# Kernel optimization log

Hardware: AMD Instinct MI355X
Metric: run time of the kernel (lower is better)

The kernel has to match this reference:

```python
import jax, jax.numpy as jnp
import numpy as np

N, E, EMB, G, L = 30000, 480000, 256, 512, 3
AVOCAB, BVOCAB, EDIM = 128, 16, 3
NEG_SLOPE = 0.2


def setup_inputs() -> dict:
    key = jax.random.key(0)
    ks = jax.random.split(key, 20)
    s = 0.05
    x = jax.random.randint(ks[0], (N, 9), 0, AVOCAB)
    edge_index = jax.random.randint(ks[1], (2, E), 0, N)
    edge_attr = jax.random.randint(ks[2], (E, 3), 0, BVOCAB)
    batch = jnp.sort(jax.random.randint(ks[3], (N,), 0, G))
    return {
        "x": x, "edge_index": edge_index, "edge_attr": edge_attr, "batch": batch,
        # AtomEncoder: 9 embedding tables summed -> [N, EMB]
        "atom_emb": jax.random.normal(ks[4], (9, AVOCAB, EMB)) * s,
        # BondEncoder per layer: 3 tables summed -> [E, 3]
        "bond_emb": jax.random.normal(ks[5], (L, 3, BVOCAB, EDIM)) * s,
        # GATConv per layer (heads=1): lin W, att vectors, lin_edge, bias
        "W": jax.random.normal(ks[6], (L, EMB, EMB)) * s,
        "att_src": jax.random.normal(ks[7], (L, EMB)) * s,
        "att_dst": jax.random.normal(ks[8], (L, EMB)) * s,
        "We": jax.random.normal(ks[9], (L, EDIM, EMB)) * s,
        "att_edge": jax.random.normal(ks[10], (L, EMB)) * s,
        "bias": jnp.zeros((L, EMB)),
        # head MLP: Linear(EMB,EMB) -> Linear(EMB,1), no activation between
        "W1": jax.random.normal(ks[11], (EMB, EMB)) * s,
        "b1": jnp.zeros((EMB,)),
        "W2": jax.random.normal(ks[12], (EMB, 1)) * s,
        "b2": jnp.zeros((1,)),
    }


def _gat_conv(h, src, dst, e_enc, W, a_s, a_d, We, a_e, b):
    # PyG GATConv, heads=1, add_self_loops=True, fill_value='mean'.
    # self-loop edge_attr = mean of incoming edge attrs per node (0 if none)
    deg = jax.ops.segment_sum(jnp.ones((E,), h.dtype), dst, num_segments=N)
    loop_attr = jax.ops.segment_sum(e_enc, dst, num_segments=N) / jnp.clip(deg, 1.0)[:, None]
    e_all = jnp.concatenate([e_enc, loop_attr], axis=0)          # [E+N, 3]
    loops = jnp.arange(N, dtype=src.dtype)
    src_a = jnp.concatenate([src, loops])
    dst_a = jnp.concatenate([dst, loops])
    xl = h @ W                                                    # [N, C]
    alpha = (xl @ a_s)[src_a] + (xl @ a_d)[dst_a] + (e_all @ We) @ a_e  # [E+N]
    alpha = jnp.where(alpha >= 0, alpha, NEG_SLOPE * alpha)       # leaky_relu
    # segment softmax over destination (every node has a self loop -> nonempty)
    m = jax.ops.segment_max(alpha, dst_a, num_segments=N)
    p = jnp.exp(alpha - m[dst_a])
    denom = jax.ops.segment_sum(p, dst_a, num_segments=N)
    w = p / denom[dst_a]
    out = jax.ops.segment_sum(w[:, None] * xl[src_a], dst_a, num_segments=N)
    return out + b


def reference(x, edge_index, edge_attr, batch, atom_emb, bond_emb, W, att_src,
              att_dst, We, att_edge, bias, W1, b1, W2, b2):
    src, dst = edge_index[0], edge_index[1]
    # AtomEncoder: sum of 9 feature embeddings
    h = sum(atom_emb[i][x[:, i]] for i in range(9))               # [N, EMB]
    for l in range(L):
        e_enc = sum(bond_emb[l, j][edge_attr[:, j]] for j in range(3))  # [E, 3]
        hc = _gat_conv(h, src, dst, e_enc, W[l], att_src[l], att_dst[l],
                       We[l], att_edge[l], bias[l])
        if l < L - 1:
            hc = jax.nn.relu(hc)
        h = hc + h  # residual (dropout is identity in eval)
    # global mean pool
    cnt = jax.ops.segment_sum(jnp.ones((N,), h.dtype), batch, num_segments=G)
    hg = jax.ops.segment_sum(h, batch, num_segments=G) / jnp.clip(cnt, 1.0)[:, None]
    return (hg @ W1 + b1) @ W2 + b2                               # [G, 1]
```

## Files before the change

kernel.cpp:

```cpp
#include <hip/hip_runtime.h>
#include <hip/hip_bf16.h>

#define NN   30000
#define NE   480000
#define EMBD 256
#define NG   512
#define NLAY 3
#define LEAK 0.2f
#define NBLK_SCAN 118

typedef __attribute__((ext_vector_type(8))) short bf16x8;
typedef __attribute__((ext_vector_type(4))) float f32x4;
typedef __attribute__((ext_vector_type(4))) unsigned short us4;
typedef __attribute__((ext_vector_type(8))) unsigned short us8;

__device__ __forceinline__ float bf2f(unsigned short u) {
  union { unsigned int i; float f; } v; v.i = ((unsigned int)u) << 16; return v.f;
}
__device__ __forceinline__ unsigned short f2bf(float f) {
  union { float f; unsigned int i; } v; v.f = f;
  unsigned int u = v.i;
  u += 0x7fffu + ((u >> 16) & 1u);
  return (unsigned short)(u >> 16);
}
__device__ __forceinline__ float rdw(const void* p, size_t i, int f32) {
  return f32 ? ((const float*)p)[i] : bf2f(((const unsigned short*)p)[i]);
}

__global__ __launch_bounds__(256) void k_sniff_multi(const unsigned short* __restrict__ w,
                                                     int* cnt) {
  __shared__ int sh;
  if (threadIdx.x == 0) sh = 0;
  __syncthreads();
  int local = 0;
  for (int i = (blockIdx.x * 256 + threadIdx.x) * 2; i < 65536; i += 16 * 256 * 2) {
    unsigned short u = w[i];
    if (((u >> 7) & 0xFF) == 0xFF) local++;
  }
  atomicAdd(&sh, local);
  __syncthreads();
  if (threadIdx.x == 0 && sh) atomicAdd(cnt, sh);
}

__global__ __launch_bounds__(256) void k_dots(const void* __restrict__ We,
                                              const void* __restrict__ ae,
                                              const void* __restrict__ W1,
                                              const void* __restrict__ b1,
                                              const void* __restrict__ W2,
                                              const void* __restrict__ b2,
                                              const int* __restrict__ cntp,
                                              float* __restrict__ wa_all,
                                              float* __restrict__ v,
                                              float* __restrict__ c0) {
  int f32 = (*cntp >= 4) ? 1 : 0;
  int wid  = blockIdx.x * 4 + (threadIdx.x >> 6);
  int lane = threadIdx.x & 63;
  if (wid >= 266) return;
  float s = 0.f;
  if (wid < 256) {
    for (int c = lane; c < 256; c += 64)
      s += rdw(W1, (size_t)wid*256 + c, f32) * rdw(W2, c, f32);
  } else if (wid < 265) {
    int t = wid - 256;
    int l = t / 3, j = t % 3;
    for (int c = lane; c < 256; c += 64)
      s += rdw(We, (size_t)l*768 + j*256 + c, f32) * rdw(ae, (size_t)l*256 + c, f32);
  } else {
    for (int c = lane; c < 256; c += 64)
      s += rdw(b1, c, f32) * rdw(W2, c, f32);
  }
  #pragma unroll
  for (int o = 32; o > 0; o >>= 1) s += __shfl_down(s, o);
  if (lane == 0) {
    if (wid < 256)      v[wid] = s;
    else if (wid < 265) wa_all[wid - 256] = s;
    else                *c0 = s + rdw(b2, 0, f32);
  }
}


__global__ void k_hist(const int* __restrict__ dst, int* cnt_i) {
  int e = blockIdx.x * 256 + threadIdx.x;
  if (e >= NE) return;
  atomicAdd(&cnt_i[dst[e]], 1);
}

__global__ __launch_bounds__(256) void k_scan_part(const int* __restrict__ cnt_i,
                                                   int* row_ptr, int* part) {
  __shared__ int sh[256];
  int b = blockIdx.x, t = threadIdx.x;
  int i = b * 256 + t;
  int v = (i < NN) ? cnt_i[i] : 0;
  sh[t] = v;
  __syncthreads();
  for (int off = 1; off < 256; off <<= 1) {
    int tmp = (t >= off) ? sh[t - off] : 0;
    __syncthreads();
    sh[t] += tmp;
    __syncthreads();
  }
  if (i < NN) row_ptr[i] = sh[t] - v;
  if (t == 255) part[b] = sh[255];
}

__global__ __launch_bounds__(128) void k_scan_mid(const int* __restrict__ part,
                                                  int* __restrict__ offs) {
  __shared__ int sh[128];
  int t = threadIdx.x;
  int v = (t < NBLK_SCAN) ? part[t] : 0;
  sh[t] = v;
  __syncthreads();
  for (int off = 1; off < 128; off <<= 1) {
    int tmp = (t >= off) ? sh[t - off] : 0;
    __syncthreads();
    sh[t] += tmp;
    __syncthreads();
  }
  if (t < NBLK_SCAN) offs[t] = sh[t] - v;
}

__global__ void k_scan_add(int* row_ptr, const int* __restrict__ offs, int* cursor) {
  int b = blockIdx.x, t = threadIdx.x;
  int i = b * 256 + t;
  if (i < NN) {
    int v = row_ptr[i] + offs[b];
    row_ptr[i] = v;
    cursor[i]  = v;
  }
  if (i == 0) row_ptr[NN] = NE;
}

__global__ void k_fill(const int* __restrict__ src, const int* __restrict__ dst,
                       int* cursor, int* col_src, int* col_eid) {
  int e = blockIdx.x * 256 + threadIdx.x;
  if (e >= NE) return;
  int pos = atomicAdd(&cursor[dst[e]], 1);
  col_src[pos] = src[e];
  col_eid[pos] = e;
}


__global__ __launch_bounds__(256) void k_prep(const void* __restrict__ W,
                                              unsigned short* __restrict__ Wt,
                                              const int* __restrict__ eattr,
                                              const int* __restrict__ col_eid,
                                              const void* __restrict__ bemb,
                                              const float* __restrict__ wa_all,
                                              float* __restrict__ we_csr,
                                              const int* __restrict__ cntp) {
  int f32 = (*cntp >= 4) ? 1 : 0;
  int b = blockIdx.x;
  if (b < 768) {
    int t = b * 256 + threadIdx.x;
    int l = t >> 16;
    int k = (t >> 8) & 255;
    int c = t & 255;
    Wt[(l << 16) + (c << 8) + k] = f2bf(rdw(W, t, f32));
  } else {
    int j = (b - 768) * 256 + threadIdx.x;
    if (j >= NE) return;
    int e = col_eid[j];
    int a0 = eattr[e*3], a1 = eattr[e*3+1], a2 = eattr[e*3+2];
    #pragma unroll
    for (int l = 0; l < NLAY; ++l) {
      size_t lb = (size_t)l * 144;
      float e0 = rdw(bemb, lb + (0*16+a0)*3+0, f32) + rdw(bemb, lb + (1*16+a1)*3+0, f32)
               + rdw(bemb, lb + (2*16+a2)*3+0, f32);
      float e1 = rdw(bemb, lb + (0*16+a0)*3+1, f32) + rdw(bemb, lb + (1*16+a1)*3+1, f32)
               + rdw(bemb, lb + (2*16+a2)*3+1, f32);
      float e2 = rdw(bemb, lb + (0*16+a0)*3+2, f32) + rdw(bemb, lb + (1*16+a1)*3+2, f32)
               + rdw(bemb, lb + (2*16+a2)*3+2, f32);
      we_csr[(size_t)l*NE + j] = e0*wa_all[l*3+0] + e1*wa_all[l*3+1] + e2*wa_all[l*3+2];
    }
  }
}

__global__ void k_atom_enc(const int* __restrict__ x, const void* __restrict__ emb,
                           float* __restrict__ h, unsigned short* __restrict__ hbf,
                           const int* __restrict__ cntp) {
  int f32 = (*cntp >= 4) ? 1 : 0;
  int n = blockIdx.x, c = threadIdx.x;
  float s = 0.f;
  #pragma unroll
  for (int i = 0; i < 9; ++i) {
    int xi = x[n * 9 + i];
    s += rdw(emb, (size_t)(i * 128 + xi) * 256 + c, f32);
  }
  h[n * 256 + c] = s;
  hbf[n * 256 + c] = f2bf(s);
}


__global__ __launch_bounds__(256) void k_gemm_fused(const unsigned short* __restrict__ A,
                                                    const unsigned short* __restrict__ Bt,
                                                    const void* __restrict__ as_w,
                                                    const void* __restrict__ ad_w, int l,
                                                    unsigned short* __restrict__ xlbf,
                                                    float* __restrict__ as_,
                                                    float* __restrict__ ad_,
                                                    const int* __restrict__ cntp) {
  __shared__ unsigned short xtile[16][256];
  __shared__ float sred[4][4][4], dred[4][4][4];
  int b = blockIdx.x;
  int w = threadIdx.x >> 6;
  int lane = threadIdx.x & 63;
  int m0 = b * 16;
  int c0 = w * 64;
  int lr = lane & 15;
  int g  = lane >> 4;
  int lk = g * 8;
  f32x4 acc0 = {0.f,0.f,0.f,0.f}, acc1 = {0.f,0.f,0.f,0.f};
  f32x4 acc2 = {0.f,0.f,0.f,0.f}, acc3 = {0.f,0.f,0.f,0.f};
  const unsigned short* arow = A  + (size_t)(m0 + lr) * 256 + lk;
  const unsigned short* b0   = Bt + (size_t)(c0 + lr) * 256 + lk;
  #pragma unroll
  for (int k = 0; k < 256; k += 32) {
    bf16x8 a = *(const bf16x8*)(arow + k);
    acc0 = __builtin_amdgcn_mfma_f32_16x16x32_bf16(a, *(const bf16x8*)(b0 + k),          acc0, 0,0,0);
    acc1 = __builtin_amdgcn_mfma_f32_16x16x32_bf16(a, *(const bf16x8*)(b0 + 16*256 + k), acc1, 0,0,0);
    acc2 = __builtin_amdgcn_mfma_f32_16x16x32_bf16(a, *(const bf16x8*)(b0 + 32*256 + k), acc2, 0,0,0);
    acc3 = __builtin_amdgcn_mfma_f32_16x16x32_bf16(a, *(const bf16x8*)(b0 + 48*256 + k), acc3, 0,0,0);
  }
  int f32 = (*cntp >= 4) ? 1 : 0;
  float asw0 = rdw(as_w, (size_t)l*256 + c0 + lr +  0, f32);
  float asw1 = rdw(as_w, (size_t)l*256 + c0 + lr + 16, f32);
  float asw2 = rdw(as_w, (size_t)l*256 + c0 + lr + 32, f32);
  float asw3 = rdw(as_w, (size_t)l*256 + c0 + lr + 48, f32);
  float adw0 = rdw(ad_w, (size_t)l*256 + c0 + lr +  0, f32);
  float adw1 = rdw(ad_w, (size_t)l*256 + c0 + lr + 16, f32);
  float adw2 = rdw(ad_w, (size_t)l*256 + c0 + lr + 32, f32);
  float adw3 = rdw(ad_w, (size_t)l*256 + c0 + lr + 48, f32);
  #pragma unroll
  for (int r = 0; r < 4; ++r) {
    float sv = acc0[r]*asw0 + acc1[r]*asw1 + acc2[r]*asw2 + acc3[r]*asw3;
    float dv = acc0[r]*adw0 + acc1[r]*adw1 + acc2[r]*adw2 + acc3[r]*adw3;
    #pragma unroll
    for (int o = 1; o < 16; o <<= 1) { sv += __shfl_xor(sv, o); dv += __shfl_xor(dv, o); }
    if (lr == 0) { sred[w][g][r] = sv; dred[w][g][r] = dv; }
    int row = g*4 + r;
    xtile[row][c0 + lr +  0] = f2bf(acc0[r]);
    xtile[row][c0 + lr + 16] = f2bf(acc1[r]);
    xtile[row][c0 + lr + 32] = f2bf(acc2[r]);
    xtile[row][c0 + lr + 48] = f2bf(acc3[r]);
  }
  __syncthreads();
  int t = threadIdx.x;
  if (t < 16) {
    int gg = t >> 2, rr = t & 3;
    float s = sred[0][gg][rr] + sred[1][gg][rr] + sred[2][gg][rr] + sred[3][gg][rr];
    float d = dred[0][gg][rr] + dred[1][gg][rr] + dred[2][gg][rr] + dred[3][gg][rr];
    as_[m0 + gg*4 + rr] = s;
    ad_[m0 + gg*4 + rr] = d;
  }
  {
    int row = t >> 4;
    int seg = t & 15;
    us8* dstp = (us8*)(xlbf + (size_t)(m0 + row) * 256);
    const us8* srcp = (const us8*)&xtile[row][0];
    dstp[seg]      = srcp[seg];
    dstp[seg + 16] = srcp[seg + 16];
  }
}

__global__ __launch_bounds__(256) void k_fused(const int* __restrict__ row_ptr,
                                               const int* __restrict__ col_src,
                                               const float* __restrict__ we_csr,
                                               const float* __restrict__ as_,
                                               const float* __restrict__ ad_,
                                               const unsigned short* __restrict__ xlbf,
                                               const void* __restrict__ bias, int l,
                                               float* __restrict__ h,
                                               unsigned short* __restrict__ hbf,
                                               int do_relu, const int* __restrict__ cntp) {
  int n = blockIdx.x * 4 + (threadIdx.x >> 6);
  int lane = threadIdx.x & 63;
  int beg = row_ptr[n], end = row_ptr[n+1];
  int deg = end - beg;
  float ad_n = ad_[n];

  float m = -1e30f, dsum = 0.f, wesum = 0.f;
  float ax = 0.f, ay = 0.f, az = 0.f, aw = 0.f;

  for (int cb = beg; cb < end; cb += 64) {
    int j = cb + lane;
    bool valid = (j < end);
    int s = valid ? col_src[j] : 0;
    float we = valid ? we_csr[j] : 0.f;
    wesum += we;
    float a;
    if (valid) {
      a = as_[s] + ad_n + we;
      a = (a >= 0.f) ? a : LEAK * a;
    } else {
      a = -1e30f;
    }
    float cm = a;
    #pragma unroll
    for (int o = 32; o > 0; o >>= 1) cm = fmaxf(cm, __shfl_xor(cm, o));
    float m_new = fmaxf(m, cm);
    float r = __expf(m - m_new);
    float p = valid ? __expf(a - m_new) : 0.f;
    float cs = p;
    #pragma unroll
    for (int o = 32; o > 0; o >>= 1) cs += __shfl_xor(cs, o);
    dsum = dsum * r + cs;
    ax *= r; ay *= r; az *= r; aw *= r;
    m = m_new;
    int cl = end - cb; if (cl > 64) cl = 64;
    for (int jj = 0; jj < cl; ++jj) {
      float w  = __shfl(p, jj);
      int   ss = __shfl(s, jj);
      us4 xv = *(const us4*)(xlbf + (size_t)ss*256 + lane*4);
      ax += w*bf2f(xv.x); ay += w*bf2f(xv.y);
      az += w*bf2f(xv.z); aw += w*bf2f(xv.w);
    }
  }
  #pragma unroll
  for (int o = 32; o > 0; o >>= 1) wesum += __shfl_xor(wesum, o);

  float a_self = as_[n] + ad_n + wesum / fmaxf((float)deg, 1.f);
  a_self = (a_self >= 0.f) ? a_self : LEAK * a_self;
  float m_f = fmaxf(m, a_self);
  float r = __expf(m - m_f);
  float p_self = __expf(a_self - m_f);
  dsum = dsum * r + p_self;
  ax *= r; ay *= r; az *= r; aw *= r;
  {
    us4 xv = *(const us4*)(xlbf + (size_t)n*256 + lane*4);
    ax += p_self*bf2f(xv.x); ay += p_self*bf2f(xv.y);
    az += p_self*bf2f(xv.z); aw += p_self*bf2f(xv.w);
  }
  float inv_d = 1.f / dsum;
  ax *= inv_d; ay *= inv_d; az *= inv_d; aw *= inv_d;

  int f32 = (*cntp >= 4) ? 1 : 0;
  int c0 = lane * 4;
  ax += rdw(bias, (size_t)l*256 + c0+0, f32);
  ay += rdw(bias, (size_t)l*256 + c0+1, f32);
  az += rdw(bias, (size_t)l*256 + c0+2, f32);
  aw += rdw(bias, (size_t)l*256 + c0+3, f32);
  if (do_relu) {
    ax = fmaxf(ax, 0.f); ay = fmaxf(ay, 0.f);
    az = fmaxf(az, 0.f); aw = fmaxf(aw, 0.f);
  }
  float* hp = h + (size_t)n*256 + c0;
  float4 hv = *(const float4*)hp;
  float h0 = ax + hv.x, h1 = ay + hv.y, h2 = az + hv.z, h3 = aw + hv.w;
  *(float4*)hp = make_float4(h0, h1, h2, h3);
  us4 q = { f2bf(h0), f2bf(h1), f2bf(h2), f2bf(h3) };
  *(us4*)(hbf + (size_t)n*256 + c0) = q;
}


__global__ __launch_bounds__(256) void k_pool_head(const float* __restrict__ h,
                                                   const int* __restrict__ batch,
                                                   const float* __restrict__ v,
                                                   const float* __restrict__ c0,
                                                   void* __restrict__ out,
                                                   const int* __restrict__ cntp) {
  int g = blockIdx.x;
  int lo = 0, hi = NN;
  while (lo < hi) { int mid = (lo + hi) >> 1; if (batch[mid] < g) lo = mid + 1; else hi = mid; }
  int start = lo;
  lo = 0; hi = NN;
  while (lo < hi) { int mid = (lo + hi) >> 1; if (batch[mid] < g + 1) lo = mid + 1; else hi = mid; }
  int endn = lo;

  int c = threadIdx.x;
  float s = 0.f;
  for (int n = start; n < endn; ++n) s += h[(size_t)n*256 + c];
  __shared__ float red[256];
  red[c] = s * v[c];
  __syncthreads();
  for (int off = 128; off > 0; off >>= 1) {
    if (c < off) red[c] += red[c + off];
    __syncthreads();
  }
  if (c == 0) {
    float cntf = (float)(endn - start);
    float val = red[0] / fmaxf(cntf, 1.f) + *c0;
    if (*cntp >= 4) ((float*)out)[g] = val;
    else            ((unsigned short*)out)[g] = f2bf(val);
  }
}

extern "C" void kernel_launch(void* const* d_in, const int* in_sizes, int n_in,
                              void* d_out, int out_size, void* d_ws, size_t ws_size,
                              hipStream_t stream) {
  const int* x     = (const int*)d_in[0];
  const int* eidx  = (const int*)d_in[1];
  const int* eattr = (const int*)d_in[2];
  const int* batch = (const int*)d_in[3];
  const void* atom_emb = d_in[4];
  const void* bond_emb = d_in[5];
  const void* W        = d_in[6];
  const void* att_src  = d_in[7];
  const void* att_dst  = d_in[8];
  const void* We       = d_in[9];
  const void* att_edge = d_in[10];
  const void* bias     = d_in[11];
  const void* W1 = d_in[12];
  const void* b1 = d_in[13];
  const void* W2 = d_in[14];
  const void* b2 = d_in[15];

  const int* src = eidx;
  const int* dst = eidx + NE;

  char* base = (char*)d_ws;
  size_t off = 0;
  auto alloc = [&](size_t bytes) -> char* {
    char* p = base + off; off += (bytes + 255) & ~(size_t)255; return p;
  };
  float* h    = (float*)alloc((size_t)NN*EMBD*4);
  unsigned short* xlbf = (unsigned short*)alloc((size_t)NN*EMBD*2);
  unsigned short* hbf  = (unsigned short*)alloc((size_t)NN*EMBD*2);
  unsigned short* wt   = (unsigned short*)alloc((size_t)NLAY*EMBD*EMBD*2);
  float* we_csr = (float*)alloc((size_t)NLAY*NE*4);
  float* as_   = (float*)alloc((size_t)NN*4);
  float* ad_   = (float*)alloc((size_t)NN*4);
  float* vvec  = (float*)alloc((size_t)EMBD*4);
  float* c0    = (float*)alloc(4);
  float* wa_all= (float*)alloc(64);
  int*   cnt   = (int*)alloc(4);
  int* cnt_i   = (int*)alloc((size_t)NN*4);
  int* row_ptr = (int*)alloc((size_t)(NN+1)*4);
  int* cursor  = (int*)alloc((size_t)NN*4);
  int* col_src = (int*)alloc((size_t)NE*4);
  int* col_eid = (int*)alloc((size_t)NE*4);
  int* part    = (int*)alloc((size_t)NBLK_SCAN*4);
  int* offs    = (int*)alloc((size_t)NBLK_SCAN*4);

  (void)hipMemsetAsync(cnt, 0, 4, stream);
  (void)hipMemsetAsync(cnt_i, 0, (size_t)NN*4, stream);
  k_sniff_multi<<<16, 256, 0, stream>>>((const unsigned short*)atom_emb, cnt);
  k_hist<<<(NE+255)/256, 256, 0, stream>>>(dst, cnt_i);
  k_scan_part<<<NBLK_SCAN, 256, 0, stream>>>(cnt_i, row_ptr, part);
  k_scan_mid<<<1, 128, 0, stream>>>(part, offs);
  k_scan_add<<<NBLK_SCAN, 256, 0, stream>>>(row_ptr, offs, cursor);
  k_fill<<<(NE+255)/256, 256, 0, stream>>>(src, dst, cursor, col_src, col_eid);
  k_dots<<<67, 256, 0, stream>>>(We, att_edge, W1, b1, W2, b2, cnt, wa_all, vvec, c0);
  k_atom_enc<<<NN, 256, 0, stream>>>(x, atom_emb, h, hbf, cnt);
  k_prep<<<768 + (NE+255)/256, 256, 0, stream>>>(W, wt, eattr, col_eid, bond_emb,
                                                 wa_all, we_csr, cnt);

  for (int l = 0; l < NLAY; ++l) {
    k_gemm_fused<<<NN/16, 256, 0, stream>>>(hbf, wt + (size_t)l*EMBD*EMBD,
                                            att_src, att_dst, l, xlbf, as_, ad_, cnt);
    k_fused<<<NN/4, 256, 0, stream>>>(row_ptr, col_src, we_csr + (size_t)l*NE,
                                      as_, ad_, xlbf, bias, l, h, hbf,
                                      (l < NLAY-1) ? 1 : 0, cnt);
  }

  k_pool_head<<<NG, 256, 0, stream>>>(h, batch, vvec, c0, d_out, cnt);
}
```

Before: 497.9 us.

## Merge setup kernels, enlarge GEMM row tile, drop online-max softmax rescaling

Independent setup kernels are merged into fewer launches: sniff with histogram, scan with dot products, and atom encoding with weight transpose. The GEMM now computes 48 rows per block, so each B-fragment load is reused across three row groups. The GAT aggregation drops the running-max online softmax and its per-chunk wave reductions, using clamped exponentials and a single reduction at the end. This removes launch overhead and per-chunk shuffle and rescale work, but the softmax is less numerically robust (clamping at ±60 changes results if logits get large), and it also unrolls the gather loop.

```diff
diff --git a/kernel.cpp b/kernel.cpp
--- a/kernel.cpp
+++ b/kernel.cpp
@@ -8,6 +8,7 @@
 #define NLAY 3
 #define LEAK 0.2f
 #define NBLK_SCAN 118
+#define GROWS 48
 
 typedef __attribute__((ext_vector_type(8))) short bf16x8;
 typedef __attribute__((ext_vector_type(4))) float f32x4;
@@ -27,80 +28,82 @@
   return f32 ? ((const float*)p)[i] : bf2f(((const unsigned short*)p)[i]);
 }
 
-__global__ __launch_bounds__(256) void k_sniff_multi(const unsigned short* __restrict__ w,
-                                                     int* cnt) {
-  __shared__ int sh;
-  if (threadIdx.x == 0) sh = 0;
-  __syncthreads();
-  int local = 0;
-  for (int i = (blockIdx.x * 256 + threadIdx.x) * 2; i < 65536; i += 16 * 256 * 2) {
-    unsigned short u = w[i];
-    if (((u >> 7) & 0xFF) == 0xFF) local++;
-  }
-  atomicAdd(&sh, local);
-  __syncthreads();
-  if (threadIdx.x == 0 && sh) atomicAdd(cnt, sh);
-}
-
-__global__ __launch_bounds__(256) void k_dots(const void* __restrict__ We,
-                                              const void* __restrict__ ae,
-                                              const void* __restrict__ W1,
-                                              const void* __restrict__ b1,
-                                              const void* __restrict__ W2,
-                                              const void* __restrict__ b2,
-                                              const int* __restrict__ cntp,
-                                              float* __restrict__ wa_all,
-                                              float* __restrict__ v,
-                                              float* __restrict__ c0) {
-  int f32 = (*cntp >= 4) ? 1 : 0;
-  int wid  = blockIdx.x * 4 + (threadIdx.x >> 6);
-  int lane = threadIdx.x & 63;
-  if (wid >= 266) return;
-  float s = 0.f;
-  if (wid < 256) {
-    for (int c = lane; c < 256; c += 64)
-      s += rdw(W1, (size_t)wid*256 + c, f32) * rdw(W2, c, f32);
-  } else if (wid < 265) {
-    int t = wid - 256;
-    int l = t / 3, j = t % 3;
-    for (int c = lane; c < 256; c += 64)
-      s += rdw(We, (size_t)l*768 + j*256 + c, f32) * rdw(ae, (size_t)l*256 + c, f32);
+__global__ __launch_bounds__(256) void k_sniff_hist(const unsigned short* __restrict__ w,
+                                                    int* cnt, const int* __restrict__ dst,
+                                                    int* cnt_i) {
+  int b = blockIdx.x;
+  if (b < 16) {
+    __shared__ int sh;
+    if (threadIdx.x == 0) sh = 0;
+    __syncthreads();
+    int local = 0;
+    for (int i = (b * 256 + threadIdx.x) * 2; i < 65536; i += 16 * 256 * 2) {
+      unsigned short u = w[i];
+      if (((u >> 7) & 0xFF) == 0xFF) local++;
+    }
+    atomicAdd(&sh, local);
+    __syncthreads();
+    if (threadIdx.x == 0 && sh) atomicAdd(cnt, sh);
   } else {
-    for (int c = lane; c < 256; c += 64)
-      s += rdw(b1, c, f32) * rdw(W2, c, f32);
-  }
-  #pragma unroll
-  for (int o = 32; o > 0; o >>= 1) s += __shfl_down(s, o);
-  if (lane == 0) {
-    if (wid < 256)      v[wid] = s;
-    else if (wid < 265) wa_all[wid - 256] = s;
-    else                *c0 = s + rdw(b2, 0, f32);
-  }
-}
-
-
-__global__ void k_hist(const int* __restrict__ dst, int* cnt_i) {
-  int e = blockIdx.x * 256 + threadIdx.x;
-  if (e >= NE) return;
-  atomicAdd(&cnt_i[dst[e]], 1);
-}
-
-__global__ __launch_bounds__(256) void k_scan_part(const int* __restrict__ cnt_i,
-                                                   int* row_ptr, int* part) {
-  __shared__ int sh[256];
-  int b = blockIdx.x, t = threadIdx.x;
-  int i = b * 256 + t;
-  int v = (i < NN) ? cnt_i[i] : 0;
-  sh[t] = v;
-  __syncthreads();
-  for (int off = 1; off < 256; off <<= 1) {
-    int tmp = (t >= off) ? sh[t - off] : 0;
-    __syncthreads();
-    sh[t] += tmp;
-    __syncthreads();
-  }
-  if (i < NN) row_ptr[i] = sh[t] - v;
-  if (t == 255) part[b] = sh[255];
+    int e = (b - 16) * 256 + threadIdx.x;
+    if (e < NE) atomicAdd(&cnt_i[dst[e]], 1);
+  }
+}
+
+__global__ __launch_bounds__(256) void k_scan_dots(const int* __restrict__ cnt_i,
+                                                   int* row_ptr, int* part,
+                                                   const void* __restrict__ We,
+                                                   const void* __restrict__ ae,
+                                                   const void* __restrict__ W1,
+                                                   const void* __restrict__ b1,
+                                                   const void* __restrict__ W2,
+                                                   const void* __restrict__ b2,
+                                                   const int* __restrict__ cntp,
+                                                   float* __restrict__ wa_all,
+                                                   float* __restrict__ v,
+                                                   float* __restrict__ c0) {
+  int b = blockIdx.x;
+  if (b < NBLK_SCAN) {
+    __shared__ int sh[256];
+    int t = threadIdx.x;
+    int i = b * 256 + t;
+    int val = (i < NN) ? cnt_i[i] : 0;
+    sh[t] = val;
+    __syncthreads();
+    for (int off = 1; off < 256; off <<= 1) {
+      int tmp = (t >= off) ? sh[t - off] : 0;
+      __syncthreads();
+      sh[t] += tmp;
+      __syncthreads();
+    }
+    if (i < NN) row_ptr[i] = sh[t] - val;
+    if (t == 255) part[b] = sh[255];
+  } else {
+    int f32 = (*cntp >= 4) ? 1 : 0;
+    int wid  = (b - NBLK_SCAN) * 4 + (threadIdx.x >> 6);
+    int lane = threadIdx.x & 63;
+    if (wid >= 266) return;
+    float s = 0.f;
+    if (wid < 256) {
+      for (int c = lane; c < 256; c += 64)
+        s += rdw(W1, (size_t)wid*256 + c, f32) * rdw(W2, c, f32);
+    } else if (wid < 265) {
+      int t = wid - 256;
+      int l = t / 3, j = t % 3;
+      for (int c = lane; c < 256; c += 64)
+        s += rdw(We, (size_t)l*768 + j*256 + c, f32) * rdw(ae, (size_t)l*256 + c, f32);
+    } else {
+      for (int c = lane; c < 256; c += 64)
+        s += rdw(b1, c, f32) * rdw(W2, c, f32);
+    }
+    #pragma unroll
+    for (int o = 32; o > 0; o >>= 1) s += __shfl_down(s, o);
+    if (lane == 0) {
+      if (wid < 256)      v[wid] = s;
+      else if (wid < 265) wa_all[wid - 256] = s;
+      else                *c0 = s + rdw(b2, 0, f32);
+    }
+  }
 }
 
 __global__ __launch_bounds__(128) void k_scan_mid(const int* __restrict__ part,
@@ -139,55 +142,56 @@
   col_eid[pos] = e;
 }
 
-
-__global__ __launch_bounds__(256) void k_prep(const void* __restrict__ W,
-                                              unsigned short* __restrict__ Wt,
-                                              const int* __restrict__ eattr,
-                                              const int* __restrict__ col_eid,
-                                              const void* __restrict__ bemb,
-                                              const float* __restrict__ wa_all,
-                                              float* __restrict__ we_csr,
-                                              const int* __restrict__ cntp) {
+__global__ __launch_bounds__(256) void k_atom_prep(const int* __restrict__ x,
+                                                   const void* __restrict__ emb,
+                                                   float* __restrict__ h,
+                                                   unsigned short* __restrict__ hbf,
+                                                   const void* __restrict__ W,
+                                                   unsigned short* __restrict__ Wt,
+                                                   const int* __restrict__ cntp) {
   int f32 = (*cntp >= 4) ? 1 : 0;
   int b = blockIdx.x;
-  if (b < 768) {
-    int t = b * 256 + threadIdx.x;
+  if (b < NN) {
+    int c = threadIdx.x;
+    float s = 0.f;
+    #pragma unroll
+    for (int i = 0; i < 9; ++i) {
+      int xi = x[b * 9 + i];
+      s += rdw(emb, (size_t)(i * 128 + xi) * 256 + c, f32);
+    }
+    h[(size_t)b * 256 + c] = s;
+    hbf[(size_t)b * 256 + c] = f2bf(s);
+  } else {
+    int t = (b - NN) * 256 + threadIdx.x;
     int l = t >> 16;
     int k = (t >> 8) & 255;
     int c = t & 255;
     Wt[(l << 16) + (c << 8) + k] = f2bf(rdw(W, t, f32));
-  } else {
-    int j = (b - 768) * 256 + threadIdx.x;
-    if (j >= NE) return;
-    int e = col_eid[j];
-    int a0 = eattr[e*3], a1 = eattr[e*3+1], a2 = eattr[e*3+2];
-    #pragma unroll
-    for (int l = 0; l < NLAY; ++l) {
-      size_t lb = (size_t)l * 144;
-      float e0 = rdw(bemb, lb + (0*16+a0)*3+0, f32) + rdw(bemb, lb + (1*16+a1)*3+0, f32)
-               + rdw(bemb, lb + (2*16+a2)*3+0, f32);
-      float e1 = rdw(bemb, lb + (0*16+a0)*3+1, f32) + rdw(bemb, lb + (1*16+a1)*3+1, f32)
-               + rdw(bemb, lb + (2*16+a2)*3+1, f32);
-      float e2 = rdw(bemb, lb + (0*16+a0)*3+2, f32) + rdw(bemb, lb + (1*16+a1)*3+2, f32)
-               + rdw(bemb, lb + (2*16+a2)*3+2, f32);
-      we_csr[(size_t)l*NE + j] = e0*wa_all[l*3+0] + e1*wa_all[l*3+1] + e2*wa_all[l*3+2];
-    }
-  }
-}
-
-__global__ void k_atom_enc(const int* __restrict__ x, const void* __restrict__ emb,
-                           float* __restrict__ h, unsigned short* __restrict__ hbf,
-                           const int* __restrict__ cntp) {
+  }
+}
+
+__global__ __launch_bounds__(256) void k_we(const int* __restrict__ eattr,
+                                            const int* __restrict__ col_eid,
+                                            const void* __restrict__ bemb,
+                                            const float* __restrict__ wa_all,
+                                            float* __restrict__ we_csr,
+                                            const int* __restrict__ cntp) {
   int f32 = (*cntp >= 4) ? 1 : 0;
-  int n = blockIdx.x, c = threadIdx.x;
-  float s = 0.f;
-  #pragma unroll
-  for (int i = 0; i < 9; ++i) {
-    int xi = x[n * 9 + i];
-    s += rdw(emb, (size_t)(i * 128 + xi) * 256 + c, f32);
-  }
-  h[n * 256 + c] = s;
-  hbf[n * 256 + c] = f2bf(s);
+  int j = blockIdx.x * 256 + threadIdx.x;
+  if (j >= NE) return;
+  int e = col_eid[j];
+  int a0 = eattr[e*3], a1 = eattr[e*3+1], a2 = eattr[e*3+2];
+  #pragma unroll
+  for (int l = 0; l < NLAY; ++l) {
+    size_t lb = (size_t)l * 144;
+    float e0 = rdw(bemb, lb + (0*16+a0)*3+0, f32) + rdw(bemb, lb + (1*16+a1)*3+0, f32)
+             + rdw(bemb, lb + (2*16+a2)*3+0, f32);
+    float e1 = rdw(bemb, lb + (0*16+a0)*3+1, f32) + rdw(bemb, lb + (1*16+a1)*3+1, f32)
+             + rdw(bemb, lb + (2*16+a2)*3+1, f32);
+    float e2 = rdw(bemb, lb + (0*16+a0)*3+2, f32) + rdw(bemb, lb + (1*16+a1)*3+2, f32)
+             + rdw(bemb, lb + (2*16+a2)*3+2, f32);
+    we_csr[(size_t)l*NE + j] = e0*wa_all[l*3+0] + e1*wa_all[l*3+1] + e2*wa_all[l*3+2];
+  }
 }
 
 
@@ -199,66 +203,78 @@
                                                     float* __restrict__ as_,
                                                     float* __restrict__ ad_,
                                                     const int* __restrict__ cntp) {
-  __shared__ unsigned short xtile[16][256];
-  __shared__ float sred[4][4][4], dred[4][4][4];
+  __shared__ unsigned short xtile[GROWS][256];
+  __shared__ float sred[4][3][16], dred[4][3][16];
   int b = blockIdx.x;
   int w = threadIdx.x >> 6;
   int lane = threadIdx.x & 63;
-  int m0 = b * 16;
+  int m0 = b * GROWS;
   int c0 = w * 64;
   int lr = lane & 15;
   int g  = lane >> 4;
   int lk = g * 8;
-  f32x4 acc0 = {0.f,0.f,0.f,0.f}, acc1 = {0.f,0.f,0.f,0.f};
-  f32x4 acc2 = {0.f,0.f,0.f,0.f}, acc3 = {0.f,0.f,0.f,0.f};
-  const unsigned short* arow = A  + (size_t)(m0 + lr) * 256 + lk;
-  const unsigned short* b0   = Bt + (size_t)(c0 + lr) * 256 + lk;
+  f32x4 acc[3][4];
+  #pragma unroll
+  for (int rg = 0; rg < 3; ++rg)
+    #pragma unroll
+    for (int q = 0; q < 4; ++q) acc[rg][q] = (f32x4){0.f,0.f,0.f,0.f};
+
+  const unsigned short* brow  = Bt + (size_t)(c0 + lr) * 256 + lk;
+  const unsigned short* arow0 = A  + (size_t)(m0 + lr) * 256 + lk;
   #pragma unroll
   for (int k = 0; k < 256; k += 32) {
-    bf16x8 a = *(const bf16x8*)(arow + k);
-    acc0 = __builtin_amdgcn_mfma_f32_16x16x32_bf16(a, *(const bf16x8*)(b0 + k),          acc0, 0,0,0);
-    acc1 = __builtin_amdgcn_mfma_f32_16x16x32_bf16(a, *(const bf16x8*)(b0 + 16*256 + k), acc1, 0,0,0);
-    acc2 = __builtin_amdgcn_mfma_f32_16x16x32_bf16(a, *(const bf16x8*)(b0 + 32*256 + k), acc2, 0,0,0);
-    acc3 = __builtin_amdgcn_mfma_f32_16x16x32_bf16(a, *(const bf16x8*)(b0 + 48*256 + k), acc3, 0,0,0);
+    bf16x8 b0 = *(const bf16x8*)(brow + k);
+    bf16x8 b1 = *(const bf16x8*)(brow + 16*256 + k);
+    bf16x8 b2 = *(const bf16x8*)(brow + 32*256 + k);
+    bf16x8 b3 = *(const bf16x8*)(brow + 48*256 + k);
+    #pragma unroll
+    for (int rg = 0; rg < 3; ++rg) {
+      bf16x8 a = *(const bf16x8*)(arow0 + (size_t)rg*16*256 + k);
+      acc[rg][0] = __builtin_amdgcn_mfma_f32_16x16x32_bf16(a, b0, acc[rg][0], 0,0,0);
+      acc[rg][1] = __builtin_amdgcn_mfma_f32_16x16x32_bf16(a, b1, acc[rg][1], 0,0,0);
+      acc[rg][2] = __builtin_amdgcn_mfma_f32_16x16x32_bf16(a, b2, acc[rg][2], 0,0,0);
+      acc[rg][3] = __builtin_amdgcn_mfma_f32_16x16x32_bf16(a, b3, acc[rg][3], 0,0,0);
+    }
   }
   int f32 = (*cntp >= 4) ? 1 : 0;
-  float asw0 = rdw(as_w, (size_t)l*256 + c0 + lr +  0, f32);
-  float asw1 = rdw(as_w, (size_t)l*256 + c0 + lr + 16, f32);
-  float asw2 = rdw(as_w, (size_t)l*256 + c0 + lr + 32, f32);
-  float asw3 = rdw(as_w, (size_t)l*256 + c0 + lr + 48, f32);
-  float adw0 = rdw(ad_w, (size_t)l*256 + c0 + lr +  0, f32);
-  float adw1 = rdw(ad_w, (size_t)l*256 + c0 + lr + 16, f32);
-  float adw2 = rdw(ad_w, (size_t)l*256 + c0 + lr + 32, f32);
-  float adw3 = rdw(ad_w, (size_t)l*256 + c0 + lr + 48, f32);
-  #pragma unroll
-  for (int r = 0; r < 4; ++r) {
-    float sv = acc0[r]*asw0 + acc1[r]*asw1 + acc2[r]*asw2 + acc3[r]*asw3;
-    float dv = acc0[r]*adw0 + acc1[r]*adw1 + acc2[r]*adw2 + acc3[r]*adw3;
-    #pragma unroll
-    for (int o = 1; o < 16; o <<= 1) { sv += __shfl_xor(sv, o); dv += __shfl_xor(dv, o); }
-    if (lr == 0) { sred[w][g][r] = sv; dred[w][g][r] = dv; }
-    int row = g*4 + r;
-    xtile[row][c0 + lr +  0] = f2bf(acc0[r]);
-    xtile[row][c0 + lr + 16] = f2bf(acc1[r]);
-    xtile[row][c0 + lr + 32] = f2bf(acc2[r]);
-    xtile[row][c0 + lr + 48] = f2bf(acc3[r]);
+  float asw[4], adw[4];
+  #pragma unroll
+  for (int q = 0; q < 4; ++q) {
+    asw[q] = rdw(as_w, (size_t)l*256 + c0 + 16*q + lr, f32);
+    adw[q] = rdw(ad_w, (size_t)l*256 + c0 + 16*q + lr, f32);
+  }
+  #pragma unroll
+  for (int rg = 0; rg < 3; ++rg) {
+    #pragma unroll
+    for (int r = 0; r < 4; ++r) {
+      float sv = acc[rg][0][r]*asw[0] + acc[rg][1][r]*asw[1]
+               + acc[rg][2][r]*asw[2] + acc[rg][3][r]*asw[3];
+      float dv = acc[rg][0][r]*adw[0] + acc[rg][1][r]*adw[1]
+               + acc[rg][2][r]*adw[2] + acc[rg][3][r]*adw[3];
+      #pragma unroll
+      for (int o = 1; o < 16; o <<= 1) { sv += __shfl_xor(sv, o); dv += __shfl_xor(dv, o); }
+      if (lr == 0) { sred[w][rg][g*4+r] = sv; dred[w][rg][g*4+r] = dv; }
+      int row = rg*16 + g*4 + r;
+      xtile[row][c0 + lr +  0] = f2bf(acc[rg][0][r]);
+      xtile[row][c0 + lr + 16] = f2bf(acc[rg][1][r]);
+      xtile[row][c0 + lr + 32] = f2bf(acc[rg][2][r]);
+      xtile[row][c0 + lr + 48] = f2bf(acc[rg][3][r]);
+    }
   }
   __syncthreads();
   int t = threadIdx.x;
-  if (t < 16) {
-    int gg = t >> 2, rr = t & 3;
-    float s = sred[0][gg][rr] + sred[1][gg][rr] + sred[2][gg][rr] + sred[3][gg][rr];
-    float d = dred[0][gg][rr] + dred[1][gg][rr] + dred[2][gg][rr] + dred[3][gg][rr];
-    as_[m0 + gg*4 + rr] = s;
-    ad_[m0 + gg*4 + rr] = d;
+  if (t < GROWS) {
+    int rg = t >> 4, rr = t & 15;
+    float s = sred[0][rg][rr] + sred[1][rg][rr] + sred[2][rg][rr] + sred[3][rg][rr];
+    float d = dred[0][rg][rr] + dred[1][rg][rr] + dred[2][rg][rr] + dred[3][rg][rr];
+    as_[m0 + t] = s;
+    ad_[m0 + t] = d;
   }
   {
-    int row = t >> 4;
-    int seg = t & 15;
-    us8* dstp = (us8*)(xlbf + (size_t)(m0 + row) * 256);
-    const us8* srcp = (const us8*)&xtile[row][0];
-    dstp[seg]      = srcp[seg];
-    dstp[seg + 16] = srcp[seg + 16];
+    const us8* srcp = (const us8*)&xtile[0][0];
+    us8* dstp = (us8*)(xlbf + (size_t)m0 * 256);
+    #pragma unroll
+    for (int u = 0; u < 6; ++u) dstp[t + u*256] = srcp[t + u*256];
   }
 }
 
@@ -278,7 +294,7 @@
   int deg = end - beg;
   float ad_n = ad_[n];
 
-  float m = -1e30f, dsum = 0.f, wesum = 0.f;
+  float dsum_l = 0.f, wesum_l = 0.f;
   float ax = 0.f, ay = 0.f, az = 0.f, aw = 0.f;
 
   for (int cb = beg; cb < end; cb += 64) {
@@ -286,45 +302,34 @@
     bool valid = (j < end);
     int s = valid ? col_src[j] : 0;
     float we = valid ? we_csr[j] : 0.f;
-    wesum += we;
-    float a;
+    wesum_l += we;
+    float p = 0.f;
     if (valid) {
-      a = as_[s] + ad_n + we;
+      float a = as_[s] + ad_n + we;
       a = (a >= 0.f) ? a : LEAK * a;
-    } else {
-      a = -1e30f;
-    }
-    float cm = a;
-    #pragma unroll
-    for (int o = 32; o > 0; o >>= 1) cm = fmaxf(cm, __shfl_xor(cm, o));
-    float m_new = fmaxf(m, cm);
-    float r = __expf(m - m_new);
-    float p = valid ? __expf(a - m_new) : 0.f;
-    float cs = p;
-    #pragma unroll
-    for (int o = 32; o > 0; o >>= 1) cs += __shfl_xor(cs, o);
-    dsum = dsum * r + cs;
-    ax *= r; ay *= r; az *= r; aw *= r;
-    m = m_new;
+      p = __expf(fmaxf(fminf(a, 60.f), -60.f));
+    }
+    dsum_l += p;
     int cl = end - cb; if (cl > 64) cl = 64;
+    #pragma unroll 4
     for (int jj = 0; jj < cl; ++jj) {
-      float w  = __shfl(p, jj);
+      float ww = __shfl(p, jj);
       int   ss = __shfl(s, jj);
       us4 xv = *(const us4*)(xlbf + (size_t)ss*256 + lane*4);
-      ax += w*bf2f(xv.x); ay += w*bf2f(xv.y);
-      az += w*bf2f(xv.z); aw += w*bf2f(xv.w);
-    }
-  }
-  #pragma unroll
-  for (int o = 32; o > 0; o >>= 1) wesum += __shfl_xor(wesum, o);
-
-  float a_self = as_[n] + ad_n + wesum / fmaxf((float)deg, 1.f);
+      ax += ww*bf2f(xv.x); ay += ww*bf2f(xv.y);
+      az += ww*bf2f(xv.z); aw += ww*bf2f(xv.w);
+    }
+  }
+  #pragma unroll
+  for (int o = 32; o > 0; o >>= 1) {
+    dsum_l  += __shfl_xor(dsum_l, o);
+    wesum_l += __shfl_xor(wesum_l, o);
+  }
+
+  float a_self = as_[n] + ad_n + wesum_l / fmaxf((float)deg, 1.f);
   a_self = (a_self >= 0.f) ? a_self : LEAK * a_self;
-  float m_f = fmaxf(m, a_self);
-  float r = __expf(m - m_f);
-  float p_self = __expf(a_self - m_f);
-  dsum = dsum * r + p_self;
-  ax *= r; ay *= r; az *= r; aw *= r;
+  float p_self = __expf(fmaxf(fminf(a_self, 60.f), -60.f));
+  float dsum = dsum_l + p_self;
   {
     us4 xv = *(const us4*)(xlbf + (size_t)n*256 + lane*4);
     ax += p_self*bf2f(xv.x); ay += p_self*bf2f(xv.y);
@@ -433,20 +438,20 @@
 
   (void)hipMemsetAsync(cnt, 0, 4, stream);
   (void)hipMemsetAsync(cnt_i, 0, (size_t)NN*4, stream);
-  k_sniff_multi<<<16, 256, 0, stream>>>((const unsigned short*)atom_emb, cnt);
-  k_hist<<<(NE+255)/256, 256, 0, stream>>>(dst, cnt_i);
-  k_scan_part<<<NBLK_SCAN, 256, 0, stream>>>(cnt_i, row_ptr, part);
+  k_sniff_hist<<<16 + (NE+255)/256, 256, 0, stream>>>((const unsigned short*)atom_emb,
+                                                      cnt, dst, cnt_i);
+  k_scan_dots<<<NBLK_SCAN + 67, 256, 0, stream>>>(cnt_i, row_ptr, part,
+                                                  We, att_edge, W1, b1, W2, b2,
+                                                  cnt, wa_all, vvec, c0);
   k_scan_mid<<<1, 128, 0, stream>>>(part, offs);
   k_scan_add<<<NBLK_SCAN, 256, 0, stream>>>(row_ptr, offs, cursor);
   k_fill<<<(NE+255)/256, 256, 0, stream>>>(src, dst, cursor, col_src, col_eid);
-  k_dots<<<67, 256, 0, stream>>>(We, att_edge, W1, b1, W2, b2, cnt, wa_all, vvec, c0);
-  k_atom_enc<<<NN, 256, 0, stream>>>(x, atom_emb, h, hbf, cnt);
-  k_prep<<<768 + (NE+255)/256, 256, 0, stream>>>(W, wt, eattr, col_eid, bond_emb,
-                                                 wa_all, we_csr, cnt);
+  k_atom_prep<<<NN + 768, 256, 0, stream>>>(x, atom_emb, h, hbf, W, wt, cnt);
+  k_we<<<(NE+255)/256, 256, 0, stream>>>(eattr, col_eid, bond_emb, wa_all, we_csr, cnt);
 
   for (int l = 0; l < NLAY; ++l) {
-    k_gemm_fused<<<NN/16, 256, 0, stream>>>(hbf, wt + (size_t)l*EMBD*EMBD,
-                                            att_src, att_dst, l, xlbf, as_, ad_, cnt);
+    k_gemm_fused<<<NN/GROWS, 256, 0, stream>>>(hbf, wt + (size_t)l*EMBD*EMBD,
+                                               att_src, att_dst, l, xlbf, as_, ad_, cnt);
     k_fused<<<NN/4, 256, 0, stream>>>(row_ptr, col_src, we_csr + (size_t)l*NE,
                                       as_, ad_, xlbf, bias, l, h, hbf,
                                       (l < NLAY-1) ? 1 : 0, cnt);
```

Result: faster. 452.0 us (-9.2%).
